# Kernel optimization log

Hardware: AMD Instinct MI355X
Metric: run time of the kernel (lower is better)

## Reference

```python
import jax, jax.numpy as jnp
import numpy as np

B, E, V, T, NSTEP = 32, 256, 32000, 2048, 128  # batch, embed_dim, graph_dim, total_length, min_len


def setup_inputs() -> dict:
    key = jax.random.key(0)
    k1, k2, k3, k4 = jax.random.split(key, 4)
    latent = jax.random.normal(k1, (T, E * E), dtype=jnp.float32) * 0.02
    vocab_w = jax.random.normal(k2, (E, V), dtype=jnp.float32) * 0.02
    vocab_b = jnp.zeros((V,), dtype=jnp.float32)
    zi = jax.random.randint(k3, (B,), 0, T)
    y = jax.random.randint(k4, (B, NSTEP), 0, V)
    return {"latent": latent, "vocab_w": vocab_w, "vocab_b": vocab_b, "zi": zi, "y": y}


def _trajectory(z_flat, n_step):
    # z_flat: [B, E*E] -> per-sample transition matrix [B, E, E]
    trans = z_flat.reshape(-1, E, E)
    z0 = trans[:, 0, :]  # seed state = first row, [B, E]

    def step(z, _):
        # torch .std() is unbiased (ddof=1)
        zn = z / (1e-5 + jnp.std(z, axis=-1, keepdims=True, ddof=1)) * 0.113
        emit = jnp.einsum('be,bef->bf', zn, trans)  # [B, E]
        return emit, emit

    _, zs = jax.lax.scan(step, z0, None, length=n_step)  # [n_step, B, E]
    return jnp.transpose(zs, (1, 0, 2))  # [B, n_step, E]


def reference(latent, vocab_w, vocab_b, zi, y):
    z = latent[zi]                      # [B, E*E]
    zs = _trajectory(z, NSTEP)          # [B, n_step, E]
    logits = zs @ vocab_w + vocab_b     # [B, n_step, V]
    logp = jax.nn.log_softmax(logits, axis=-1)
    yp = jnp.take_along_axis(logp, y[..., None], axis=-1)[..., 0]  # [B, n_step]
    return yp
```

## Files before the change

### kernel.cpp

```cpp
#include <hip/hip_runtime.h>
#include <hip/hip_bf16.h>

#define BATCH 32
#define E 256
#define V 32000
#define NSTEP 128
#define M_TOTAL (BATCH * NSTEP)
#define BM 128
#define BN2 128
#define NBT (V / BN2)
#define NGRP 8
#define L2E 1.4426950408889634f

typedef __attribute__((ext_vector_type(4))) float f32x4;
typedef __attribute__((ext_vector_type(2))) float f32x2;
typedef __attribute__((ext_vector_type(8))) short s16x8;
typedef __attribute__((ext_vector_type(4))) unsigned int u32x4;

static __device__ __forceinline__ short f2bf(float v) {
    __hip_bfloat16 h = __float2bfloat16(v);
    return *reinterpret_cast<short*>(&h);
}

static __device__ __forceinline__ unsigned char f2fp8(float v) {
    int p = __builtin_amdgcn_cvt_pk_fp8_f32(v, v, 0, false);
    return (unsigned char)(p & 0xff);
}
template<bool HI>
static __device__ __forceinline__ f32x2 fp8x2_to_f32(unsigned int x) {
    return __builtin_amdgcn_cvt_pk_f32_fp8((int)x, HI);
}

static __device__ __forceinline__ int fragpos(int e) {
    return ((e >> 3) & 3) * 64 + (e >> 5) * 8 + (e & 7);
}

static __device__ __forceinline__ long long ll2(unsigned int a, unsigned int b) {
    return (long long)(((unsigned long long)b << 32) | a);
}

static __device__ __forceinline__ void gload_lds16(const void* g, void* l) {
    __builtin_amdgcn_global_load_lds((const __attribute__((address_space(1))) void*)g,
                                     (__attribute__((address_space(3))) void*)l,
                                     16, 0, 0);
}

template<int CTRL>
static __device__ __forceinline__ float dpp_add(float v) {
    int i = __builtin_amdgcn_update_dpp(0, __builtin_bit_cast(int, v), CTRL, 0xF, 0xF, false);
    return v + __builtin_bit_cast(float, i);
}
static __device__ __forceinline__ float row16_sum(float v) {
    v = dpp_add<0x121>(v);
    v = dpp_add<0x122>(v);
    v = dpp_add<0x124>(v);
    v = dpp_add<0x128>(v);
    return v;
}

__global__ __launch_bounds__(512, 2) void traj_transpose_kernel(
        const float* __restrict__ latent, const int* __restrict__ zi,
        const float* __restrict__ w,
        unsigned char* __restrict__ zsb8, unsigned char* __restrict__ wt8) {
    __shared__ float tile[64][65];
    __shared__ __align__(16) short zsh[2][E];
    __shared__ __align__(16) float red[2][16];

    const int tid = threadIdx.x;

    if (blockIdx.x >= BATCH) {
        const int bb = blockIdx.x - BATCH;
        const int k0 = (bb & 3) * 64;
        const int n0 = (bb >> 2) * 64;
        const int c  = tid & 63;
        const int r8 = tid >> 6;
        #pragma unroll
        for (int r = r8; r < 64; r += 8)
            tile[r][c] = w[(size_t)(k0 + r) * V + n0 + c];
        __syncthreads();
        const int fp = fragpos(k0 + c);
        #pragma unroll
        for (int r = r8; r < 64; r += 8)
            wt8[(size_t)(n0 + r) * E + fp] = f2fp8(tile[c][r]);
        return;
    }

    const int b    = blockIdx.x;
    const int lane = tid & 63;
    const int wv   = tid >> 6;
    const int lm   = lane & 15;
    const int g    = lane >> 4;
    const float* tr = latent + (size_t)zi[b] * (E * E);

    s16x8 bfrag[2][8];
    #pragma unroll
    for (int nt = 0; nt < 2; ++nt)
        #pragma unroll
        for (int kk = 0; kk < 8; ++kk) {
            s16x8 fr;
            #pragma unroll
            for (int j = 0; j < 8; ++j)
                fr[j] = f2bf(tr[(size_t)(kk * 32 + g * 8 + j) * E + wv * 32 + nt * 16 + lm]);
            bfrag[nt][kk] = fr;
        }

    if (tid < E) zsh[0][tid] = f2bf(tr[tid]);

    {
        float v = (tid < E) ? tr[tid] : 0.f;
        float a = row16_sum(v), a2 = row16_sum(v * v);
        a  += __shfl_xor(a, 16);  a2 += __shfl_xor(a2, 16);
        a  += __shfl_xor(a, 32);  a2 += __shfl_xor(a2, 32);
        if (lane == 0) { red[1][wv] = a; red[1][8 + wv] = a2; }
    }
    __syncthreads();

    float scale_prev = 1.0f;

    const int p0i = fragpos(wv * 32 + lm);
    const int p1i = fragpos(wv * 32 + 16 + lm);

    for (int tb = 0; tb < NSTEP; tb += 8) {
        unsigned char eb0[8], eb1[8];

        #pragma unroll
        for (int s = 0; s < 8; ++s) {
            const int t = tb + s;
            const short* zrd = zsh[t & 1];
            s16x8 a[8];
            #pragma unroll
            for (int kk = 0; kk < 8; ++kk)
                a[kk] = *(const s16x8*)((const char*)zrd + kk * 64 + g * 16);

            const float* rd = red[(t + 1) & 1];
            f32x4 q0 = *(const f32x4*)&rd[0], q1 = *(const f32x4*)&rd[4];
            f32x4 v0 = *(const f32x4*)&rd[8], v1 = *(const f32x4*)&rd[12];
            float ts  = (q0[0]+q0[1]+q0[2]+q0[3]) + (q1[0]+q1[1]+q1[2]+q1[3]);
            float ts2 = (v0[0]+v0[1]+v0[2]+v0[3]) + (v1[0]+v1[1]+v1[2]+v1[3]);
            float var = fmaxf((ts2 - ts * ts * (1.0f / 256.0f)) * (1.0f / 255.0f), 0.f);
            const float scale_cur = 0.113f / (1e-5f + scale_prev * sqrtf(var));

            f32x4 a0l = {}, a0h = {}, a1l = {}, a1h = {};
            #pragma unroll
            for (int kk = 0; kk < 4; ++kk) {
                a0l = __builtin_amdgcn_mfma_f32_16x16x32_bf16(a[kk], bfrag[0][kk], a0l, 0, 0, 0);
                a1l = __builtin_amdgcn_mfma_f32_16x16x32_bf16(a[kk], bfrag[1][kk], a1l, 0, 0, 0);
            }
            #pragma unroll
            for (int kk = 4; kk < 8; ++kk) {
                a0h = __builtin_amdgcn_mfma_f32_16x16x32_bf16(a[kk], bfrag[0][kk], a0h, 0, 0, 0);
                a1h = __builtin_amdgcn_mfma_f32_16x16x32_bf16(a[kk], bfrag[1][kk], a1h, 0, 0, 0);
            }

            const float u0 = scale_prev * (a0l[0] + a0h[0]);
            const float u1 = scale_prev * (a1l[0] + a1h[0]);
            if (g == 0) {
                zsh[(t + 1) & 1][wv * 32 + lm]      = f2bf(u0);
                zsh[(t + 1) & 1][wv * 32 + 16 + lm] = f2bf(u1);
                eb0[s] = f2fp8(scale_cur * u0);
                eb1[s] = f2fp8(scale_cur * u1);
            }

            float su  = row16_sum(u0 + u1);
            float su2 = row16_sum(u0 * u0 + u1 * u1);
            if (lane == 0) { red[t & 1][wv] = su; red[t & 1][8 + wv] = su2; }

            scale_prev = scale_cur;
            __syncthreads();
        }

        if (g == 0) {
            unsigned char* zr = zsb8 + ((size_t)b * NSTEP + tb) * E;
            #pragma unroll
            for (int s = 0; s < 8; ++s) {
                zr[s * E + p0i] = eb0[s];
                zr[s * E + p1i] = eb1[s];
            }
        }
    }
}

__global__ __launch_bounds__(512, 2) void gemm_lse_kernel(const unsigned char* __restrict__ zsb8,
                                                          const unsigned char* __restrict__ wt8,
                                                          const float* __restrict__ vb,
                                                          float* __restrict__ partial) {
    __shared__ unsigned char bpan0[BN2 * E];
    __shared__ unsigned char bpan1[BN2 * E];

    const int tid  = threadIdx.x;
    const int lane = tid & 63;
    const int w    = tid >> 6;
    const int grp  = blockIdx.x & 7;
    const int bm   = blockIdx.x >> 3;
    const int m0   = bm * BM;
    const int t0   = (NBT * grp) >> 3;
    const int t1   = (NBT * (grp + 1)) >> 3;

    const int wr = w >> 2, wc = w & 3;
    const int lm = lane & 15, lk = lane >> 4;
    const int mw = m0 + wr * 64;

    long long areg[4][8];
    #pragma unroll
    for (int rt = 0; rt < 4; ++rt)
        #pragma unroll
        for (int kp = 0; kp < 4; ++kp) {
            u32x4 v = *(const u32x4*)(zsb8 + (size_t)(mw + rt * 16 + lm) * E + lk * 64 + kp * 16);
            areg[rt][2 * kp]     = ll2(v[0], v[1]);
            areg[rt][2 * kp + 1] = ll2(v[2], v[3]);
        }

    float rs[4][4] = {};

    auto STAGE = [&](int tile, unsigned char* dst) {
        const size_t gbase = (size_t)(tile * BN2) * E;
        #pragma unroll
        for (int j = 0; j < 4; ++j) {
            const int c   = j * 512 + tid;
            const int row = c >> 4;
            const int gsl = ((c & 15) - row) & 15;
            gload_lds16(wt8 + gbase + (size_t)row * E + gsl * 16, dst + c * 16);
        }
    };

    auto COMPUTE = [&](const unsigned char* bp, f32x4 (&acc)[4][2], float (&bias)[2], int tile) {
        const int n0 = tile * BN2;
        bias[0] = vb[n0 + wc * 32 + lm] * L2E;
        bias[1] = vb[n0 + wc * 32 + 16 + lm] * L2E;
        #pragma unroll
        for (int rt = 0; rt < 4; ++rt) { acc[rt][0] = (f32x4){}; acc[rt][1] = (f32x4){}; }
        #pragma unroll
        for (int kp = 0; kp < 4; ++kp) {
            long long blo[2], bhi[2];
            #pragma unroll
            for (int nt = 0; nt < 2; ++nt) {
                const int rn   = wc * 32 + nt * 16 + lm;
                const int slot = (lk * 4 + kp + rn) & 15;
                u32x4 bv = *(const u32x4*)(bp + rn * 256 + slot * 16);
                blo[nt] = ll2(bv[0], bv[1]);
                bhi[nt] = ll2(bv[2], bv[3]);
            }
            #pragma unroll
            for (int rt = 0; rt < 4; ++rt) {
                acc[rt][0] = __builtin_amdgcn_mfma_f32_16x16x32_fp8_fp8(areg[rt][2 * kp], blo[0], acc[rt][0], 0, 0, 0);
                acc[rt][1] = __builtin_amdgcn_mfma_f32_16x16x32_fp8_fp8(areg[rt][2 * kp], blo[1], acc[rt][1], 0, 0, 0);
            }
            #pragma unroll
            for (int rt = 0; rt < 4; ++rt) {
                acc[rt][0] = __builtin_amdgcn_mfma_f32_16x16x32_fp8_fp8(areg[rt][2 * kp + 1], bhi[0], acc[rt][0], 0, 0, 0);
                acc[rt][1] = __builtin_amdgcn_mfma_f32_16x16x32_fp8_fp8(areg[rt][2 * kp + 1], bhi[1], acc[rt][1], 0, 0, 0);
            }
        }
    };

    auto EPI = [&](const f32x4 (&acc)[4][2], const float (&bias)[2]) {
        #pragma unroll
        for (int rt = 0; rt < 4; ++rt)
            #pragma unroll
            for (int r = 0; r < 4; ++r)
                rs[rt][r] += __builtin_amdgcn_exp2f(acc[rt][0][r] * L2E + bias[0])
                           + __builtin_amdgcn_exp2f(acc[rt][1][r] * L2E + bias[1]);
    };

    f32x4 accA[4][2], accB[4][2];
    float biasA[2], biasB[2];

    STAGE(t0, bpan0);
    __syncthreads();
    if (t0 + 1 < t1) STAGE(t0 + 1, bpan1);
    COMPUTE(bpan0, accA, biasA, t0);
    __syncthreads();

    int i = t0 + 1;
    bool lastA = true;
    while (i < t1) {
        {
            const unsigned char* bp = ((i - t0) & 1) ? bpan1 : bpan0;
            unsigned char*       st = ((i - t0) & 1) ? bpan0 : bpan1;
            if (i + 1 < t1) STAGE(i + 1, st);
            COMPUTE(bp, accB, biasB, i);
            EPI(accA, biasA);
            __syncthreads();
            lastA = false; ++i;
            if (i >= t1) break;
        }
        {
            const unsigned char* bp = ((i - t0) & 1) ? bpan1 : bpan0;
            unsigned char*       st = ((i - t0) & 1) ? bpan0 : bpan1;
            if (i + 1 < t1) STAGE(i + 1, st);
            COMPUTE(bp, accA, biasA, i);
            EPI(accB, biasB);
            __syncthreads();
            lastA = true; ++i;
        }
    }
    if (lastA) EPI(accA, biasA); else EPI(accB, biasB);

    const int cr = lane >> 4;
    #pragma unroll
    for (int rt = 0; rt < 4; ++rt)
        #pragma unroll
        for (int r = 0; r < 4; ++r) {
            const float v = row16_sum(rs[rt][r]);
            if (lm == 0)
                partial[(size_t)(grp * 4 + wc) * M_TOTAL + mw + rt * 16 + cr * 4 + r] = v;
        }
}

__global__ __launch_bounds__(256) void finalize_kernel(const unsigned char* __restrict__ zsb8,
                                                       const unsigned char* __restrict__ wt8,
                                                       const float* __restrict__ vb,
                                                       const int* __restrict__ y,
                                                       const float* __restrict__ partial,
                                                       float* __restrict__ out) {
    const int tid  = threadIdx.x;
    const int lane = tid & 63;
    const int rw   = lane >> 4;
    const int kl   = lane & 15;
    const int row  = blockIdx.x * 16 + (tid >> 6) * 4 + rw;
    const int yrow = y[row];

    u32x4 za = *(const u32x4*)(zsb8 + (size_t)row * E + kl * 16);
    u32x4 wa = *(const u32x4*)(wt8 + (size_t)yrow * E + kl * 16);
    float acc = 0.f;
    #pragma unroll
    for (int q = 0; q < 4; ++q) {
        f32x2 a0 = fp8x2_to_f32<false>(za[q]), b0 = fp8x2_to_f32<false>(wa[q]);
        f32x2 a1 = fp8x2_to_f32<true>(za[q]),  b1 = fp8x2_to_f32<true>(wa[q]);
        acc += a0[0] * b0[0] + a0[1] * b0[1] + a1[0] * b1[0] + a1[1] * b1[1];
    }
    const float logit = row16_sum(acc) + vb[yrow];

    float ps = partial[(size_t)kl * M_TOTAL + row] + partial[(size_t)(kl + 16) * M_TOTAL + row];
    const float tot = row16_sum(ps);

    if (kl == 0) out[row] = logit - logf(tot);
}

extern "C" void kernel_launch(void* const* d_in, const int* in_sizes, int n_in,
                              void* d_out, int out_size, void* d_ws, size_t ws_size,
                              hipStream_t stream) {
    const float* latent  = (const float*)d_in[0];
    const float* vocab_w = (const float*)d_in[1];
    const float* vocab_b = (const float*)d_in[2];
    const int*   zi      = (const int*)d_in[3];
    const int*   y       = (const int*)d_in[4];
    float* out = (float*)d_out;

    char* ws = (char*)d_ws;
    float*         partial = (float*)(ws);
    unsigned char* zsb8    = (unsigned char*)(ws + 524288);
    unsigned char* wt8     = (unsigned char*)(ws + 524288 + 1048576);

    hipLaunchKernelGGL(traj_transpose_kernel, dim3(BATCH + 4 * (V / 64)), dim3(512), 0, stream,
                       latent, zi, vocab_w, zsb8, wt8);
    hipLaunchKernelGGL(gemm_lse_kernel, dim3(32 * NGRP), dim3(512), 0, stream,
                       zsb8, wt8, vocab_b, partial);
    hipLaunchKernelGGL(finalize_kernel, dim3(M_TOTAL / 16), dim3(256), 0, stream,
                       zsb8, wt8, vocab_b, y, partial, out);
}
```

Measured before the change: 144.2 us.

## Square transition matrix to advance trajectory two steps per barrier

Precomputes the squared per-sample transition matrix (T·T) with MFMA into shared memory, then runs two interleaved chains, even and odd steps, each advancing by T² so that one synchronisation covers two recurrence steps. Normalisation scales are carried algebraically across the chains, which halves the number of serial barrier-separated steps. In exchange it adds an upfront 256x256x256 matmul per block, a 64KB shared panel that lowers occupancy, and extra bf16 rounding from the squared matrix that may change accuracy.

```diff
diff --git a/kernel.cpp b/kernel.cpp
--- a/kernel.cpp
+++ b/kernel.cpp
@@ -62,13 +62,11 @@
         const float* __restrict__ latent, const int* __restrict__ zi,
         const float* __restrict__ w,
         unsigned char* __restrict__ zsb8, unsigned char* __restrict__ wt8) {
-    __shared__ float tile[64][65];
-    __shared__ __align__(16) short zsh[2][E];
-    __shared__ __align__(16) float red[2][16];
-
+    __shared__ __align__(16) unsigned char smem[67840];
     const int tid = threadIdx.x;
 
     if (blockIdx.x >= BATCH) {
+        float (*tile)[65] = (float(*)[65])smem;
         const int bb = blockIdx.x - BATCH;
         const int k0 = (bb & 3) * 64;
         const int n0 = (bb >> 2) * 64;
@@ -84,6 +82,11 @@
             wt8[(size_t)(n0 + r) * E + fp] = f2fp8(tile[c][r]);
         return;
     }
+
+    short* panel = (short*)smem;
+    short* uE    = (short*)(smem + 65536);
+    short* uO    = (short*)(smem + 66560);
+    float* red   = (float*)(smem + 67584);
 
     const int b    = blockIdx.x;
     const int lane = tid & 63;
@@ -92,7 +95,7 @@
     const int g    = lane >> 4;
     const float* tr = latent + (size_t)zi[b] * (E * E);
 
-    s16x8 bfrag[2][8];
+    s16x8 bfragW[2][8];
     #pragma unroll
     for (int nt = 0; nt < 2; ++nt)
         #pragma unroll
@@ -101,81 +104,164 @@
             #pragma unroll
             for (int j = 0; j < 8; ++j)
                 fr[j] = f2bf(tr[(size_t)(kk * 32 + g * 8 + j) * E + wv * 32 + nt * 16 + lm]);
-            bfrag[nt][kk] = fr;
-        }
-
-    if (tid < E) zsh[0][tid] = f2bf(tr[tid]);
-
+            bfragW[nt][kk] = fr;
+        }
+
+    if (tid < E) uE[tid] = f2bf(tr[tid]);
     {
         float v = (tid < E) ? tr[tid] : 0.f;
         float a = row16_sum(v), a2 = row16_sum(v * v);
         a  += __shfl_xor(a, 16);  a2 += __shfl_xor(a2, 16);
         a  += __shfl_xor(a, 32);  a2 += __shfl_xor(a2, 32);
-        if (lane == 0) { red[1][wv] = a; red[1][8 + wv] = a2; }
+        if (lane == 0) { red[32 + wv] = a; red[32 + 8 + wv] = a2; }
     }
     __syncthreads();
 
-    float scale_prev = 1.0f;
+    auto rsum8 = [](const float* p) -> float {
+        f32x4 x0 = *(const f32x4*)p, x1 = *(const f32x4*)(p + 4);
+        return (x0[0]+x0[1]+x0[2]+x0[3]) + (x1[0]+x1[1]+x1[2]+x1[3]);
+    };
+    auto stdev = [](float ts, float ts2) -> float {
+        return sqrtf(fmaxf((ts2 - ts * ts * (1.0f / 256.0f)) * (1.0f / 255.0f), 0.f));
+    };
+
+    float c_e;
+    {
+        float s0 = stdev(rsum8(&red[32]), rsum8(&red[32 + 8]));
+        c_e = 0.113f / (1e-5f + s0);
+    }
 
     const int p0i = fragpos(wv * 32 + lm);
     const int p1i = fragpos(wv * 32 + 16 + lm);
 
-    for (int tb = 0; tb < NSTEP; tb += 8) {
+    {
+        s16x8 a[8];
+        #pragma unroll
+        for (int kk = 0; kk < 8; ++kk)
+            a[kk] = *(const s16x8*)((const char*)uE + kk * 64 + g * 16);
+        f32x4 m0 = {}, m1 = {};
+        #pragma unroll
+        for (int kk = 0; kk < 8; ++kk) {
+            m0 = __builtin_amdgcn_mfma_f32_16x16x32_bf16(a[kk], bfragW[0][kk], m0, 0, 0, 0);
+            m1 = __builtin_amdgcn_mfma_f32_16x16x32_bf16(a[kk], bfragW[1][kk], m1, 0, 0, 0);
+        }
+        const float u1a = c_e * m0[0], u1b = c_e * m1[0];
+        if (g == 0) {
+            uO[wv * 32 + lm]      = f2bf(u1a);
+            uO[wv * 32 + 16 + lm] = f2bf(u1b);
+            unsigned char* zr = zsb8 + (size_t)b * NSTEP * E;
+            zr[p0i] = f2fp8(u1a);
+            zr[p1i] = f2fp8(u1b);
+        }
+        float su  = row16_sum(u1a + u1b);
+        float su2 = row16_sum(u1a * u1a + u1b * u1b);
+        if (lane == 0) { red[32 + 16 + wv] = su; red[32 + 24 + wv] = su2; }
+    }
+    __syncthreads();
+
+    float c_o, a_o = 1.0f;
+    {
+        float s1 = stdev(rsum8(&red[32 + 16]), rsum8(&red[32 + 24]));
+        c_o = 0.113f / (1e-5f + s1);
+    }
+
+    s16x8 bfrag2[2][8];
+    short* pan = panel + wv * 4096;
+    #pragma unroll
+    for (int jt = 0; jt < 2; ++jt) {
+        for (int it = 0; it < 16; ++it) {
+            f32x4 acc4 = {};
+            #pragma unroll
+            for (int kk = 0; kk < 8; ++kk) {
+                const float* ap = tr + (size_t)(16 * it + lm) * E + kk * 32 + g * 8;
+                f32x4 w0 = *(const f32x4*)ap, w1 = *(const f32x4*)(ap + 4);
+                s16x8 af;
+                af[0] = f2bf(w0[0]); af[1] = f2bf(w0[1]); af[2] = f2bf(w0[2]); af[3] = f2bf(w0[3]);
+                af[4] = f2bf(w1[0]); af[5] = f2bf(w1[1]); af[6] = f2bf(w1[2]); af[7] = f2bf(w1[3]);
+                acc4 = __builtin_amdgcn_mfma_f32_16x16x32_bf16(af, bfragW[jt][kk], acc4, 0, 0, 0);
+            }
+            short* pw = pan + (16 * it + g * 4) * 16;
+            pw[0 * 16 + lm] = f2bf(acc4[0]);
+            pw[1 * 16 + lm] = f2bf(acc4[1]);
+            pw[2 * 16 + lm] = f2bf(acc4[2]);
+            pw[3 * 16 + lm] = f2bf(acc4[3]);
+        }
+        #pragma unroll
+        for (int kk = 0; kk < 8; ++kk) {
+            s16x8 fr;
+            #pragma unroll
+            for (int j = 0; j < 8; ++j)
+                fr[j] = pan[(32 * kk + 8 * g + j) * 16 + lm];
+            bfrag2[jt][kk] = fr;
+        }
+    }
+
+    for (int q = 0; q < 16; ++q) {
         unsigned char eb0[8], eb1[8];
-
-        #pragma unroll
-        for (int s = 0; s < 8; ++s) {
-            const int t = tb + s;
-            const short* zrd = zsh[t & 1];
-            s16x8 a[8];
-            #pragma unroll
-            for (int kk = 0; kk < 8; ++kk)
-                a[kk] = *(const s16x8*)((const char*)zrd + kk * 64 + g * 16);
-
-            const float* rd = red[(t + 1) & 1];
-            f32x4 q0 = *(const f32x4*)&rd[0], q1 = *(const f32x4*)&rd[4];
-            f32x4 v0 = *(const f32x4*)&rd[8], v1 = *(const f32x4*)&rd[12];
-            float ts  = (q0[0]+q0[1]+q0[2]+q0[3]) + (q1[0]+q1[1]+q1[2]+q1[3]);
-            float ts2 = (v0[0]+v0[1]+v0[2]+v0[3]) + (v1[0]+v1[1]+v1[2]+v1[3]);
-            float var = fmaxf((ts2 - ts * ts * (1.0f / 256.0f)) * (1.0f / 255.0f), 0.f);
-            const float scale_cur = 0.113f / (1e-5f + scale_prev * sqrtf(var));
-
-            f32x4 a0l = {}, a0h = {}, a1l = {}, a1h = {};
-            #pragma unroll
-            for (int kk = 0; kk < 4; ++kk) {
-                a0l = __builtin_amdgcn_mfma_f32_16x16x32_bf16(a[kk], bfrag[0][kk], a0l, 0, 0, 0);
-                a1l = __builtin_amdgcn_mfma_f32_16x16x32_bf16(a[kk], bfrag[1][kk], a1l, 0, 0, 0);
-            }
-            #pragma unroll
-            for (int kk = 4; kk < 8; ++kk) {
-                a0h = __builtin_amdgcn_mfma_f32_16x16x32_bf16(a[kk], bfrag[0][kk], a0h, 0, 0, 0);
-                a1h = __builtin_amdgcn_mfma_f32_16x16x32_bf16(a[kk], bfrag[1][kk], a1h, 0, 0, 0);
-            }
-
-            const float u0 = scale_prev * (a0l[0] + a0h[0]);
-            const float u1 = scale_prev * (a1l[0] + a1h[0]);
+        #pragma unroll
+        for (int rr = 0; rr < 4; ++rr) {
+            const int p = rr & 1;
+            const short* pe = uE + p * 256;
+            const short* po = uO + p * 256;
+            s16x8 ae[8], ao[8];
+            #pragma unroll
+            for (int kk = 0; kk < 8; ++kk) {
+                ae[kk] = *(const s16x8*)((const char*)pe + kk * 64 + g * 16);
+                ao[kk] = *(const s16x8*)((const char*)po + kk * 64 + g * 16);
+            }
+
+            f32x4 e0 = {}, e1 = {}, o0 = {}, o1 = {};
+            #pragma unroll
+            for (int kk = 0; kk < 8; ++kk) {
+                e0 = __builtin_amdgcn_mfma_f32_16x16x32_bf16(ae[kk], bfrag2[0][kk], e0, 0, 0, 0);
+                e1 = __builtin_amdgcn_mfma_f32_16x16x32_bf16(ae[kk], bfrag2[1][kk], e1, 0, 0, 0);
+                o0 = __builtin_amdgcn_mfma_f32_16x16x32_bf16(ao[kk], bfrag2[0][kk], o0, 0, 0, 0);
+                o1 = __builtin_amdgcn_mfma_f32_16x16x32_bf16(ao[kk], bfrag2[1][kk], o1, 0, 0, 0);
+            }
+
+            const float fac_e = c_o * c_e;
+            const float fac_o = fac_e * a_o;
+            const float ue_a = fac_e * e0[0], ue_b = fac_e * e1[0];
+            const float uo_a = fac_o * o0[0], uo_b = fac_o * o1[0];
+
             if (g == 0) {
-                zsh[(t + 1) & 1][wv * 32 + lm]      = f2bf(u0);
-                zsh[(t + 1) & 1][wv * 32 + 16 + lm] = f2bf(u1);
-                eb0[s] = f2fp8(scale_cur * u0);
-                eb1[s] = f2fp8(scale_cur * u1);
-            }
-
-            float su  = row16_sum(u0 + u1);
-            float su2 = row16_sum(u0 * u0 + u1 * u1);
-            if (lane == 0) { red[t & 1][wv] = su; red[t & 1][8 + wv] = su2; }
-
-            scale_prev = scale_cur;
+                short* we = uE + ((p ^ 1) * 256) + wv * 32;
+                short* wo = uO + ((p ^ 1) * 256) + wv * 32;
+                we[lm] = f2bf(ue_a);  we[16 + lm] = f2bf(ue_b);
+                wo[lm] = f2bf(uo_a);  wo[16 + lm] = f2bf(uo_b);
+            }
+            float se  = row16_sum(ue_a + ue_b);
+            float se2 = row16_sum(ue_a * ue_a + ue_b * ue_b);
+            float so  = row16_sum(uo_a + uo_b);
+            float so2 = row16_sum(uo_a * uo_a + uo_b * uo_b);
+            if (lane == 0) {
+                float* rp = red + p * 32;
+                rp[wv] = se; rp[8 + wv] = se2; rp[16 + wv] = so; rp[24 + wv] = so2;
+            }
             __syncthreads();
-        }
-
+
+            const float* rp = red + p * 32;
+            const float sig_e = stdev(rsum8(&rp[0]),  rsum8(&rp[8]));
+            const float sig_o = stdev(rsum8(&rp[16]), rsum8(&rp[24]));
+            const float c_e_new = 0.113f / (1e-5f + sig_e);
+            const float a_o_new = c_e_new / c_e;
+            const float c_o_new = 0.113f / (1e-5f + a_o_new * sig_o);
+
+            eb0[rr * 2]     = f2fp8(ue_a);
+            eb1[rr * 2]     = f2fp8(ue_b);
+            eb0[rr * 2 + 1] = f2fp8(a_o_new * uo_a);
+            eb1[rr * 2 + 1] = f2fp8(a_o_new * uo_b);
+
+            c_e = c_e_new; c_o = c_o_new; a_o = a_o_new;
+        }
         if (g == 0) {
-            unsigned char* zr = zsb8 + ((size_t)b * NSTEP + tb) * E;
-            #pragma unroll
-            for (int s = 0; s < 8; ++s) {
-                zr[s * E + p0i] = eb0[s];
-                zr[s * E + p1i] = eb1[s];
-            }
+            unsigned char* zr = zsb8 + ((size_t)b * NSTEP + 8 * q + 1) * E;
+            #pragma unroll
+            for (int s = 0; s < 8; ++s)
+                if (8 * q + 1 + s < NSTEP) {
+                    zr[s * E + p0i] = eb0[s];
+                    zr[s * E + p1i] = eb1[s];
+                }
         }
     }
 }
```

Result: slower. 250.4 us (+73.6%).

## Halve trajectory block to 4 waves, each computing 64 output columns

Applied to the files above, without the earlier changes.

The trajectory recurrence block shrinks from 8 to 4 waves, with each wave holding 4 column tiles of the transition matrix in registers and issuing 16 MFMAs per K-half. The goal is to make each serial step's __syncthreads and cross-wave reduction cheaper by involving fewer waves. In exchange each step carries a longer MFMA chain per wave, and register pressure roughly doubles. The transpose blocks now use 256 threads with more rows per thread.

```diff
diff --git a/kernel.cpp b/kernel.cpp
--- a/kernel.cpp
+++ b/kernel.cpp
@@ -58,13 +58,13 @@
     return v;
 }
 
-__global__ __launch_bounds__(512, 2) void traj_transpose_kernel(
+__global__ __launch_bounds__(256, 1) void traj_transpose_kernel(
         const float* __restrict__ latent, const int* __restrict__ zi,
         const float* __restrict__ w,
         unsigned char* __restrict__ zsb8, unsigned char* __restrict__ wt8) {
     __shared__ float tile[64][65];
     __shared__ __align__(16) short zsh[2][E];
-    __shared__ __align__(16) float red[2][16];
+    __shared__ __align__(16) float red[2][8];
 
     const int tid = threadIdx.x;
 
@@ -73,14 +73,14 @@
         const int k0 = (bb & 3) * 64;
         const int n0 = (bb >> 2) * 64;
         const int c  = tid & 63;
-        const int r8 = tid >> 6;
-        #pragma unroll
-        for (int r = r8; r < 64; r += 8)
+        const int r4 = tid >> 6;
+        #pragma unroll
+        for (int r = r4; r < 64; r += 4)
             tile[r][c] = w[(size_t)(k0 + r) * V + n0 + c];
         __syncthreads();
         const int fp = fragpos(k0 + c);
         #pragma unroll
-        for (int r = r8; r < 64; r += 8)
+        for (int r = r4; r < 64; r += 4)
             wt8[(size_t)(n0 + r) * E + fp] = f2fp8(tile[c][r]);
         return;
     }
@@ -92,36 +92,37 @@
     const int g    = lane >> 4;
     const float* tr = latent + (size_t)zi[b] * (E * E);
 
-    s16x8 bfrag[2][8];
-    #pragma unroll
-    for (int nt = 0; nt < 2; ++nt)
+    s16x8 bfrag[4][8];
+    #pragma unroll
+    for (int nt = 0; nt < 4; ++nt)
         #pragma unroll
         for (int kk = 0; kk < 8; ++kk) {
             s16x8 fr;
             #pragma unroll
             for (int j = 0; j < 8; ++j)
-                fr[j] = f2bf(tr[(size_t)(kk * 32 + g * 8 + j) * E + wv * 32 + nt * 16 + lm]);
+                fr[j] = f2bf(tr[(size_t)(kk * 32 + g * 8 + j) * E + wv * 64 + nt * 16 + lm]);
             bfrag[nt][kk] = fr;
         }
 
-    if (tid < E) zsh[0][tid] = f2bf(tr[tid]);
+    zsh[0][tid] = f2bf(tr[tid]);
 
     {
-        float v = (tid < E) ? tr[tid] : 0.f;
+        float v = tr[tid];
         float a = row16_sum(v), a2 = row16_sum(v * v);
         a  += __shfl_xor(a, 16);  a2 += __shfl_xor(a2, 16);
         a  += __shfl_xor(a, 32);  a2 += __shfl_xor(a2, 32);
-        if (lane == 0) { red[1][wv] = a; red[1][8 + wv] = a2; }
+        if (lane == 0) { red[1][wv] = a; red[1][4 + wv] = a2; }
     }
     __syncthreads();
 
     float scale_prev = 1.0f;
 
-    const int p0i = fragpos(wv * 32 + lm);
-    const int p1i = fragpos(wv * 32 + 16 + lm);
+    int pp[4];
+    #pragma unroll
+    for (int nt = 0; nt < 4; ++nt) pp[nt] = fragpos(wv * 64 + nt * 16 + lm);
 
     for (int tb = 0; tb < NSTEP; tb += 8) {
-        unsigned char eb0[8], eb1[8];
+        unsigned char eb[4][8];
 
         #pragma unroll
         for (int s = 0; s < 8; ++s) {
@@ -133,37 +134,40 @@
                 a[kk] = *(const s16x8*)((const char*)zrd + kk * 64 + g * 16);
 
             const float* rd = red[(t + 1) & 1];
-            f32x4 q0 = *(const f32x4*)&rd[0], q1 = *(const f32x4*)&rd[4];
-            f32x4 v0 = *(const f32x4*)&rd[8], v1 = *(const f32x4*)&rd[12];
-            float ts  = (q0[0]+q0[1]+q0[2]+q0[3]) + (q1[0]+q1[1]+q1[2]+q1[3]);
-            float ts2 = (v0[0]+v0[1]+v0[2]+v0[3]) + (v1[0]+v1[1]+v1[2]+v1[3]);
+            f32x4 q = *(const f32x4*)&rd[0];
+            f32x4 v4 = *(const f32x4*)&rd[4];
+            float ts  = (q[0] + q[1]) + (q[2] + q[3]);
+            float ts2 = (v4[0] + v4[1]) + (v4[2] + v4[3]);
             float var = fmaxf((ts2 - ts * ts * (1.0f / 256.0f)) * (1.0f / 255.0f), 0.f);
             const float scale_cur = 0.113f / (1e-5f + scale_prev * sqrtf(var));
 
-            f32x4 a0l = {}, a0h = {}, a1l = {}, a1h = {};
-            #pragma unroll
-            for (int kk = 0; kk < 4; ++kk) {
-                a0l = __builtin_amdgcn_mfma_f32_16x16x32_bf16(a[kk], bfrag[0][kk], a0l, 0, 0, 0);
-                a1l = __builtin_amdgcn_mfma_f32_16x16x32_bf16(a[kk], bfrag[1][kk], a1l, 0, 0, 0);
+            f32x4 lo[4] = {}, hi[4] = {};
+            #pragma unroll
+            for (int kk = 0; kk < 4; ++kk)
+                #pragma unroll
+                for (int nt = 0; nt < 4; ++nt)
+                    lo[nt] = __builtin_amdgcn_mfma_f32_16x16x32_bf16(a[kk], bfrag[nt][kk], lo[nt], 0, 0, 0);
+            #pragma unroll
+            for (int kk = 4; kk < 8; ++kk)
+                #pragma unroll
+                for (int nt = 0; nt < 4; ++nt)
+                    hi[nt] = __builtin_amdgcn_mfma_f32_16x16x32_bf16(a[kk], bfrag[nt][kk], hi[nt], 0, 0, 0);
+
+            float u[4];
+            #pragma unroll
+            for (int nt = 0; nt < 4; ++nt) u[nt] = scale_prev * (lo[nt][0] + hi[nt][0]);
+
+            if (g == 0) {
+                #pragma unroll
+                for (int nt = 0; nt < 4; ++nt) {
+                    zsh[(t + 1) & 1][wv * 64 + nt * 16 + lm] = f2bf(u[nt]);
+                    eb[nt][s] = f2fp8(scale_cur * u[nt]);
+                }
             }
-            #pragma unroll
-            for (int kk = 4; kk < 8; ++kk) {
-                a0h = __builtin_amdgcn_mfma_f32_16x16x32_bf16(a[kk], bfrag[0][kk], a0h, 0, 0, 0);
-                a1h = __builtin_amdgcn_mfma_f32_16x16x32_bf16(a[kk], bfrag[1][kk], a1h, 0, 0, 0);
-            }
-
-            const float u0 = scale_prev * (a0l[0] + a0h[0]);
-            const float u1 = scale_prev * (a1l[0] + a1h[0]);
-            if (g == 0) {
-                zsh[(t + 1) & 1][wv * 32 + lm]      = f2bf(u0);
-                zsh[(t + 1) & 1][wv * 32 + 16 + lm] = f2bf(u1);
-                eb0[s] = f2fp8(scale_cur * u0);
-                eb1[s] = f2fp8(scale_cur * u1);
-            }
-
-            float su  = row16_sum(u0 + u1);
-            float su2 = row16_sum(u0 * u0 + u1 * u1);
-            if (lane == 0) { red[t & 1][wv] = su; red[t & 1][8 + wv] = su2; }
+
+            float su  = row16_sum((u[0] + u[1]) + (u[2] + u[3]));
+            float su2 = row16_sum((u[0] * u[0] + u[1] * u[1]) + (u[2] * u[2] + u[3] * u[3]));
+            if (lane == 0) { red[t & 1][wv] = su; red[t & 1][4 + wv] = su2; }
 
             scale_prev = scale_cur;
             __syncthreads();
@@ -172,10 +176,10 @@
         if (g == 0) {
             unsigned char* zr = zsb8 + ((size_t)b * NSTEP + tb) * E;
             #pragma unroll
-            for (int s = 0; s < 8; ++s) {
-                zr[s * E + p0i] = eb0[s];
-                zr[s * E + p1i] = eb1[s];
-            }
+            for (int s = 0; s < 8; ++s)
+                #pragma unroll
+                for (int nt = 0; nt < 4; ++nt)
+                    zr[s * E + pp[nt]] = eb[nt][s];
         }
     }
 }
@@ -352,7 +356,7 @@
     unsigned char* zsb8    = (unsigned char*)(ws + 524288);
     unsigned char* wt8     = (unsigned char*)(ws + 524288 + 1048576);
 
-    hipLaunchKernelGGL(traj_transpose_kernel, dim3(BATCH + 4 * (V / 64)), dim3(512), 0, stream,
+    hipLaunchKernelGGL(traj_transpose_kernel, dim3(BATCH + 4 * (V / 64)), dim3(256), 0, stream,
                        latent, zi, vocab_w, zsb8, wt8);
     hipLaunchKernelGGL(gemm_lse_kernel, dim3(32 * NGRP), dim3(512), 0, stream,
                        zsb8, wt8, vocab_b, partial);
```

Result: no change. 143.6 us (-0.4%).
